# Optimization experiments

Measured on AMD Instinct MI355X. Metric: run time of the kernel, lower is better.

## Reference

```python
import jax, jax.numpy as jnp
import numpy as np

N = 100000       # nodes
E = 1600000      # edges (avg degree 16)
F_IN, H, C = 128, 128, 47


def setup_inputs() -> dict:
    key = jax.random.key(0)
    ks = jax.random.split(key, 12)
    def lin(k, fan_in, fan_out):
        return (jax.random.normal(k, (fan_in, fan_out), dtype=jnp.float32)
                / np.float32(np.sqrt(fan_in)))
    return {
        "x": jax.random.normal(ks[0], (N, F_IN), dtype=jnp.float32),
        "src": jax.random.randint(ks[1], (E,), 0, N, dtype=jnp.int32),
        "dst": jax.random.randint(ks[2], (E,), 0, N, dtype=jnp.int32),
        "w_self0": lin(ks[3], F_IN, H),
        "w_neigh0": lin(ks[4], F_IN, H),
        "b0": jnp.zeros((H,), jnp.float32),
        "w_self1": lin(ks[5], H, H),
        "w_neigh1": lin(ks[6], H, H),
        "b1": jnp.zeros((H,), jnp.float32),
        "w_self2": lin(ks[7], H, C),
        "w_neigh2": lin(ks[8], H, C),
        "b2": jnp.zeros((C,), jnp.float32),
    }


def _sage_layer(h, src, dst, w_self, w_neigh, b):
    # mean-aggregate neighbor features: gather h[src], scatter-add to dst
    agg = jax.ops.segment_sum(h[src], dst, num_segments=N)        # [N, d]
    deg = jax.ops.segment_sum(jnp.ones((src.shape[0], 1), h.dtype), dst,
                              num_segments=N)                     # [N, 1]
    mean = agg / jnp.maximum(deg, 1.0)
    # DGL SAGEConv('mean'): fc_self(h_dst) + fc_neigh(mean) + bias
    return h @ w_self + mean @ w_neigh + b


def reference(x, src, dst,
              w_self0, w_neigh0, b0,
              w_self1, w_neigh1, b1,
              w_self2, w_neigh2, b2):
    h = _sage_layer(x, src, dst, w_self0, w_neigh0, b0)
    h = jax.nn.relu(h)  # dropout is identity in eval mode
    h = _sage_layer(h, src, dst, w_self1, w_neigh1, b1)
    h = jax.nn.relu(h)
    h = _sage_layer(h, src, dst, w_self2, w_neigh2, b2)
    return h
```

## Files before the change

### kernel.cpp

```cpp
#include <hip/hip_runtime.h>

typedef unsigned int u32;
typedef unsigned short u16;
typedef __attribute__((ext_vector_type(8))) short short8;
typedef __attribute__((ext_vector_type(4))) float f32x4;

__device__ __forceinline__ u16 f2bf(float f) {
    u32 u = __float_as_uint(f);
    u32 r = (u + 0x7fffu + ((u >> 16) & 1u)) >> 16;
    return (u16)r;
}
__device__ __forceinline__ float bf2f(u32 lo16) { return __uint_as_float(lo16 << 16); }

__device__ __forceinline__ void acc_u4(float* a, uint4 v) {
    a[0] += bf2f(v.x & 0xffffu); a[1] += bf2f(v.x >> 16);
    a[2] += bf2f(v.y & 0xffffu); a[3] += bf2f(v.y >> 16);
    a[4] += bf2f(v.z & 0xffffu); a[5] += bf2f(v.z >> 16);
    a[6] += bf2f(v.w & 0xffffu); a[7] += bf2f(v.w >> 16);
}


__global__ __launch_bounds__(256) void prep_w_all(const float* __restrict__ ws0, const float* __restrict__ wn0, u16* __restrict__ wt0,
                                                  const float* __restrict__ ws1, const float* __restrict__ wn1, u16* __restrict__ wt1,
                                                  const float* __restrict__ ws2, const float* __restrict__ wn2, u16* __restrict__ wt2) {
    int bid = blockIdx.x;
    const float *ws, *wn;
    u16* wt;
    int dout, HW, local;
    if (bid < 128)      { ws = ws0; wn = wn0; wt = wt0; dout = 128; HW = 128; local = bid; }
    else if (bid < 256) { ws = ws1; wn = wn1; wt = wt1; dout = 128; HW = 128; local = bid - 128; }
    else                { ws = ws2; wn = wn2; wt = wt2; dout = 47;  HW = 64;  local = bid - 256; }
    int idx = local * 256 + threadIdx.x;
    int n = idx >> 7, k = idx & 127;
    float v = 0.f;
    if (n < HW) { if (n < dout) v = ws[k * dout + n]; }
    else { int nn = n - HW; if (nn < dout) v = wn[k * dout + nn]; }
    wt[idx] = f2bf(v);
}


__global__ __launch_bounds__(256) void hist_k(const int* __restrict__ dst,
                                              int* __restrict__ deg, int E) {
    int i = blockIdx.x * 256 + threadIdx.x;
    if (i < E) atomicAdd(&deg[dst[i]], 1);
}

__global__ __launch_bounds__(256) void scan_partial(const int* __restrict__ deg,
                                                    int* __restrict__ bsum, int Nn) {
    __shared__ int sm[256];
    int t = threadIdx.x;
    int base = blockIdx.x * 1024 + t * 4;
    int s = 0;
#pragma unroll
    for (int j = 0; j < 4; j++)
        if (base + j < Nn) s += deg[base + j];
    sm[t] = s;
    __syncthreads();
    for (int off = 128; off > 0; off >>= 1) {
        if (t < off) sm[t] += sm[t + off];
        __syncthreads();
    }
    if (t == 0) bsum[blockIdx.x] = sm[0];
}

__global__ __launch_bounds__(256) void scan_offsets(const int* __restrict__ bsum,
                                                    int* __restrict__ boff, int nb) {
    __shared__ int sm[256];
    int t = threadIdx.x;
    int v = (t < nb) ? bsum[t] : 0;
    sm[t] = v;
    __syncthreads();
    for (int off = 1; off < 256; off <<= 1) {
        int u = (t >= off) ? sm[t - off] : 0;
        __syncthreads();
        sm[t] += u;
        __syncthreads();
    }
    if (t < nb) boff[t] = sm[t] - v;
}

__global__ __launch_bounds__(1024) void scan_final(const int* __restrict__ deg,
                                                   const int* __restrict__ boff,
                                                   int* __restrict__ rowptr,
                                                   float* __restrict__ invd,
                                                   int* __restrict__ cursor,
                                                   int Nn, int E) {
    __shared__ int sm[1024];
    int t = threadIdx.x;
    int i = blockIdx.x * 1024 + t;
    int v = (i < Nn) ? deg[i] : 0;
    sm[t] = v;
    __syncthreads();
    for (int off = 1; off < 1024; off <<= 1) {
        int u = (t >= off) ? sm[t - off] : 0;
        __syncthreads();
        sm[t] += u;
        __syncthreads();
    }
    if (i < Nn) {
        int rp = boff[blockIdx.x] + sm[t] - v;
        rowptr[i] = rp;
        invd[i] = 1.0f / (float)max(v, 1);
        if ((i & 511) == 0) cursor[i >> 9] = rp;
    }
    if (i == Nn) rowptr[Nn] = E;
}

#define TILE 4096
__global__ __launch_bounds__(512) void bucket_scatter(const int* __restrict__ src,
                                                      const int* __restrict__ dst,
                                                      int* __restrict__ cursor,
                                                      uint2* __restrict__ pairs, int E) {
    __shared__ uint2 sp[TILE];
    __shared__ int s_cnt[256], s_off[256], s_gpos[256], s_cnt2[256];
    const int tid = threadIdx.x;
    const int base = blockIdx.x * TILE;
    const int tn = min(TILE, E - base);
    if (tid < 256) { s_cnt[tid] = 0; s_cnt2[tid] = 0; }
    __syncthreads();
    int d[8], s[8];
#pragma unroll
    for (int j = 0; j < 8; j++) {
        int k = tid + j * 512;
        if (k < tn) {
            d[j] = dst[base + k];
            s[j] = src[base + k];
            atomicAdd(&s_cnt[d[j] >> 9], 1);
        } else d[j] = -1;
    }
    __syncthreads();
    if (tid < 256) s_off[tid] = s_cnt[tid];
    __syncthreads();
    for (int off = 1; off < 256; off <<= 1) {
        int v = 0;
        if (tid < 256 && tid >= off) v = s_off[tid - off];
        __syncthreads();
        if (tid < 256) s_off[tid] += v;
        __syncthreads();
    }
    if (tid < 256 && s_cnt[tid] > 0) s_gpos[tid] = atomicAdd(&cursor[tid], s_cnt[tid]);
    __syncthreads();
#pragma unroll
    for (int j = 0; j < 8; j++) {
        if (d[j] >= 0) {
            int b = d[j] >> 9;
            int p = atomicAdd(&s_cnt2[b], 1);
            sp[s_off[b] - s_cnt[b] + p] = make_uint2((u32)d[j], (u32)s[j]);
        }
    }
    __syncthreads();
    for (int k = tid; k < tn; k += 512) {
        uint2 pr = sp[k];
        int b = (int)(pr.x >> 9);
        pairs[s_gpos[b] + (k - (s_off[b] - s_cnt[b]))] = pr;
    }
}

#define LDSCAP 12288
__global__ __launch_bounds__(512) void build_csr(const uint2* __restrict__ pairs,
                                                 const int* __restrict__ rowptr,
                                                 int* __restrict__ cols, int Nn) {
    __shared__ int s_cols[LDSCAP];
    __shared__ int s_row[513];
    __shared__ int s_cnt[512];
    const int tid = threadIdx.x;
    const int d0 = blockIdx.x * 512;
    const int nd = min(512, Nn - d0);
    for (int i = tid; i <= nd; i += 512) s_row[i] = rowptr[d0 + i];
    if (tid < nd) s_cnt[tid] = 0;
    __syncthreads();
    const int base = s_row[0];
    const int n = s_row[nd] - base;
    const bool fit = (n <= LDSCAP);
    for (int k = tid; k < n; k += 512) {
        uint2 pr = pairs[base + k];
        int dl = (int)pr.x - d0;
        int p = atomicAdd(&s_cnt[dl], 1);
        int pos = s_row[dl] - base + p;
        if (fit) s_cols[pos] = (int)pr.y;
        else cols[base + pos] = (int)pr.y;
    }
    __syncthreads();
    if (fit)
        for (int k = tid; k < n; k += 512) cols[base + k] = s_cols[k];
}

#define KDIM 128
#define KP 136

template <int NCOLS, bool AF32>
__global__ __launch_bounds__(256) void gemm_bf16(const void* __restrict__ Ap,
                                                 const u16* __restrict__ Bt,
                                                 u16* __restrict__ C, int M) {
    __shared__ u16 As[64 * KP];
    __shared__ u16 Bs[128 * KP];
    const int row0 = blockIdx.x * 64;
    const int col0 = blockIdx.y * 128;
    const int tid = threadIdx.x;

#pragma unroll
    for (int i = 0; i < 4; i++) {
        int idx = tid + i * 256;
        int r = idx >> 4, c = idx & 15;
        uint4 v = make_uint4(0, 0, 0, 0);
        if (row0 + r < M) {
            if (AF32) {
                const float* Af = (const float*)Ap;
                const float4* rowp = (const float4*)(Af + (size_t)(row0 + r) * KDIM);
                float4 f0 = rowp[2 * c];
                float4 f1 = rowp[2 * c + 1];
                v.x = (u32)f2bf(f0.x) | ((u32)f2bf(f0.y) << 16);
                v.y = (u32)f2bf(f0.z) | ((u32)f2bf(f0.w) << 16);
                v.z = (u32)f2bf(f1.x) | ((u32)f2bf(f1.y) << 16);
                v.w = (u32)f2bf(f1.z) | ((u32)f2bf(f1.w) << 16);
            } else {
                const u16* Ab = (const u16*)Ap;
                v = ((const uint4*)(Ab + (size_t)(row0 + r) * KDIM))[c];
            }
        }
        ((uint4*)(As + r * KP))[c] = v;
    }
#pragma unroll
    for (int i = 0; i < 8; i++) {
        int idx = tid + i * 256;
        int r = idx >> 4, c = idx & 15;
        uint4 v = ((const uint4*)(Bt + (size_t)(col0 + r) * KDIM))[c];
        ((uint4*)(Bs + r * KP))[c] = v;
    }
    __syncthreads();

    const int lane = tid & 63, wave = tid >> 6;
    const int quad = lane >> 4, l16 = lane & 15;
    const int wcol = wave * 32;

    f32x4 acc[4][2];
#pragma unroll
    for (int mt = 0; mt < 4; mt++)
#pragma unroll
        for (int nt = 0; nt < 2; nt++) acc[mt][nt] = (f32x4){0.f, 0.f, 0.f, 0.f};

#pragma unroll
    for (int kc = 0; kc < 4; kc++) {
        short8 a[4], b[2];
#pragma unroll
        for (int mt = 0; mt < 4; mt++)
            a[mt] = *(const short8*)(As + (size_t)(mt * 16 + l16) * KP + kc * 32 + quad * 8);
#pragma unroll
        for (int nt = 0; nt < 2; nt++)
            b[nt] = *(const short8*)(Bs + (size_t)(wcol + nt * 16 + l16) * KP + kc * 32 + quad * 8);
#pragma unroll
        for (int mt = 0; mt < 4; mt++)
#pragma unroll
            for (int nt = 0; nt < 2; nt++)
                acc[mt][nt] = __builtin_amdgcn_mfma_f32_16x16x32_bf16(a[mt], b[nt], acc[mt][nt], 0, 0, 0);
    }

    __syncthreads();
#pragma unroll
    for (int mt = 0; mt < 4; mt++)
#pragma unroll
        for (int i = 0; i < 4; i++) {
            int rl = mt * 16 + quad * 4 + i;
#pragma unroll
            for (int nt = 0; nt < 2; nt++)
                As[rl * KP + wcol + nt * 16 + l16] = f2bf(acc[mt][nt][i]);
        }
    __syncthreads();
#pragma unroll
    for (int it = 0; it < 4; it++) {
        int idx = tid + it * 256;
        int r = idx >> 4, c8 = idx & 15;
        if (row0 + r < M)
            *(uint4*)(C + (size_t)(row0 + r) * NCOLS + col0 + c8 * 8) =
                *(const uint4*)(As + r * KP + c8 * 8);
    }
}

template <bool RELU>
__global__ __launch_bounds__(256) void agg128_k(const u16* __restrict__ out2,
                                                const int* __restrict__ rowptr,
                                                const int* __restrict__ cols,
                                                const float* __restrict__ invd,
                                                const float* __restrict__ bias,
                                                u16* __restrict__ outp, int Mn) {
    int wave = threadIdx.x >> 6, lane = threadIdx.x & 63;
    int nA = blockIdx.x * 8 + wave * 2;
    if (nA >= Mn) return;
    const int nB = nA + 1;
    const bool hasB = (nB < Mn);
    int sub = lane >> 4, l16 = lane & 15;
    const u16* tb = out2 + 128 + 8 * l16;
    int begA = rowptr[nA], endA = rowptr[nA + 1];
    int begB = 0, endB = 0;
    if (hasB) { begB = rowptr[nB]; endB = rowptr[nB + 1]; }
    float aA[8] = {0.f, 0.f, 0.f, 0.f, 0.f, 0.f, 0.f, 0.f};
    float aB[8] = {0.f, 0.f, 0.f, 0.f, 0.f, 0.f, 0.f, 0.f};
    int eA = begA + sub, eB = begB + sub;
    while (eA < endA || eB < endB) {
        bool pA0 = eA < endA, pA1 = eA + 4 < endA;
        bool pB0 = eB < endB, pB1 = eB + 4 < endB;
        int sA0 = pA0 ? cols[eA] : 0;
        int sA1 = pA1 ? cols[eA + 4] : 0;
        int sB0 = pB0 ? cols[eB] : 0;
        int sB1 = pB1 ? cols[eB + 4] : 0;
        uint4 vA0 = *(const uint4*)(tb + (size_t)sA0 * 256);
        uint4 vA1 = *(const uint4*)(tb + (size_t)sA1 * 256);
        uint4 vB0 = *(const uint4*)(tb + (size_t)sB0 * 256);
        uint4 vB1 = *(const uint4*)(tb + (size_t)sB1 * 256);
        if (!pA0) vA0 = make_uint4(0, 0, 0, 0);
        if (!pA1) vA1 = make_uint4(0, 0, 0, 0);
        if (!pB0) vB0 = make_uint4(0, 0, 0, 0);
        if (!pB1) vB1 = make_uint4(0, 0, 0, 0);
        acc_u4(aA, vA0); acc_u4(aA, vA1);
        acc_u4(aB, vB0); acc_u4(aB, vB1);
        eA += 8; eB += 8;
    }
#pragma unroll
    for (int j = 0; j < 8; j++) {
        aA[j] += __shfl_xor(aA[j], 16); aA[j] += __shfl_xor(aA[j], 32);
        aB[j] += __shfl_xor(aB[j], 16); aB[j] += __shfl_xor(aB[j], 32);
    }
    if (sub == 0 || (sub == 1 && hasB)) {
        int node = (sub == 0) ? nA : nB;
        float o[8];
#pragma unroll
        for (int j = 0; j < 8; j++) o[j] = (sub == 0) ? aA[j] : aB[j];
        float id = invd[node];
        uint4 sv = *(const uint4*)(out2 + (size_t)node * 256 + 8 * l16);
        float4 b0 = *(const float4*)(bias + 8 * l16);
        float4 b1 = *(const float4*)(bias + 8 * l16 + 4);
        float o0 = bf2f(sv.x & 0xffffu) + o[0] * id + b0.x;
        float o1 = bf2f(sv.x >> 16)     + o[1] * id + b0.y;
        float o2 = bf2f(sv.y & 0xffffu) + o[2] * id + b0.z;
        float o3 = bf2f(sv.y >> 16)     + o[3] * id + b0.w;
        float o4 = bf2f(sv.z & 0xffffu) + o[4] * id + b1.x;
        float o5 = bf2f(sv.z >> 16)     + o[5] * id + b1.y;
        float o6 = bf2f(sv.w & 0xffffu) + o[6] * id + b1.z;
        float o7 = bf2f(sv.w >> 16)     + o[7] * id + b1.w;
        if (RELU) {
            o0 = fmaxf(o0, 0.f); o1 = fmaxf(o1, 0.f); o2 = fmaxf(o2, 0.f); o3 = fmaxf(o3, 0.f);
            o4 = fmaxf(o4, 0.f); o5 = fmaxf(o5, 0.f); o6 = fmaxf(o6, 0.f); o7 = fmaxf(o7, 0.f);
        }
        uint4 w;
        w.x = (u32)f2bf(o0) | ((u32)f2bf(o1) << 16);
        w.y = (u32)f2bf(o2) | ((u32)f2bf(o3) << 16);
        w.z = (u32)f2bf(o4) | ((u32)f2bf(o5) << 16);
        w.w = (u32)f2bf(o6) | ((u32)f2bf(o7) << 16);
        *(uint4*)(outp + (size_t)node * 128 + 8 * l16) = w;
    }
}

__global__ __launch_bounds__(256) void agg_out8_k(const u16* __restrict__ out2,
                                                  const int* __restrict__ rowptr,
                                                  const int* __restrict__ cols,
                                                  const float* __restrict__ invd,
                                                  const float* __restrict__ bias,
                                                  float* __restrict__ outp, int Mn) {
    int wave = threadIdx.x >> 6, lane = threadIdx.x & 63;
    int nA = blockIdx.x * 8 + wave * 2;
    if (nA >= Mn) return;
    const int nB = nA + 1;
    const bool hasB = (nB < Mn);
    int e8 = lane >> 3, l8 = lane & 7;
    const u16* tb = out2 + 64 + 8 * l8;
    int begA = rowptr[nA], endA = rowptr[nA + 1];
    int begB = 0, endB = 0;
    if (hasB) { begB = rowptr[nB]; endB = rowptr[nB + 1]; }
    float aA[8] = {0.f, 0.f, 0.f, 0.f, 0.f, 0.f, 0.f, 0.f};
    float aB[8] = {0.f, 0.f, 0.f, 0.f, 0.f, 0.f, 0.f, 0.f};
    int eA = begA + e8, eB = begB + e8;
    while (eA < endA || eB < endB) {
        bool pA0 = eA < endA, pA1 = eA + 8 < endA;
        bool pB0 = eB < endB, pB1 = eB + 8 < endB;
        int sA0 = pA0 ? cols[eA] : 0;
        int sA1 = pA1 ? cols[eA + 8] : 0;
        int sB0 = pB0 ? cols[eB] : 0;
        int sB1 = pB1 ? cols[eB + 8] : 0;
        uint4 vA0 = *(const uint4*)(tb + (size_t)sA0 * 128);
        uint4 vA1 = *(const uint4*)(tb + (size_t)sA1 * 128);
        uint4 vB0 = *(const uint4*)(tb + (size_t)sB0 * 128);
        uint4 vB1 = *(const uint4*)(tb + (size_t)sB1 * 128);
        if (!pA0) vA0 = make_uint4(0, 0, 0, 0);
        if (!pA1) vA1 = make_uint4(0, 0, 0, 0);
        if (!pB0) vB0 = make_uint4(0, 0, 0, 0);
        if (!pB1) vB1 = make_uint4(0, 0, 0, 0);
        acc_u4(aA, vA0); acc_u4(aA, vA1);
        acc_u4(aB, vB0); acc_u4(aB, vB1);
        eA += 16; eB += 16;
    }
#pragma unroll
    for (int j = 0; j < 8; j++) {
        aA[j] += __shfl_xor(aA[j], 8); aA[j] += __shfl_xor(aA[j], 16); aA[j] += __shfl_xor(aA[j], 32);
        aB[j] += __shfl_xor(aB[j], 8); aB[j] += __shfl_xor(aB[j], 16); aB[j] += __shfl_xor(aB[j], 32);
    }
    if (e8 == 0 || (e8 == 1 && hasB)) {
        int node = (e8 == 0) ? nA : nB;
        float o[8];
#pragma unroll
        for (int j = 0; j < 8; j++) o[j] = (e8 == 0) ? aA[j] : aB[j];
        float id = invd[node];
        uint4 sv = *(const uint4*)(out2 + (size_t)node * 128 + 8 * l8);
        u32 sw[4] = {sv.x, sv.y, sv.z, sv.w};
        float* orow = outp + (size_t)node * 47;
#pragma unroll
        for (int j = 0; j < 8; j++) {
            int c = 8 * l8 + j;
            if (c < 47) {
                float s = bf2f((j & 1) ? (sw[j >> 1] >> 16) : (sw[j >> 1] & 0xffffu));
                orow[c] = s + o[j] * id + bias[c];
            }
        }
    }
}


extern "C" void kernel_launch(void* const* d_in, const int* in_sizes, int n_in,
                              void* d_out, int out_size, void* d_ws, size_t ws_size,
                              hipStream_t stream) {
    const float* x   = (const float*)d_in[0];
    const int*   src = (const int*)d_in[1];
    const int*   dst = (const int*)d_in[2];
    const float* ws0 = (const float*)d_in[3];
    const float* wn0 = (const float*)d_in[4];
    const float* b0  = (const float*)d_in[5];
    const float* ws1 = (const float*)d_in[6];
    const float* wn1 = (const float*)d_in[7];
    const float* b1  = (const float*)d_in[8];
    const float* ws2 = (const float*)d_in[9];
    const float* wn2 = (const float*)d_in[10];
    const float* b2  = (const float*)d_in[11];

    const int Nn = in_sizes[0] / 128;
    const int E  = in_sizes[1];

    char* p = (char*)d_ws;
    auto alloc = [&](size_t bytes) -> void* {
        void* r = (void*)p;
        p += (bytes + 255) & ~(size_t)255;
        return r;
    };
    u16*   bufA   = (u16*)alloc((size_t)Nn * 128 * 2);
    u16*   out2   = (u16*)alloc((size_t)Nn * 256 * 2);
    u16*   wt0    = (u16*)alloc(256 * 128 * 2);
    u16*   wt1    = (u16*)alloc(256 * 128 * 2);
    u16*   wt2    = (u16*)alloc(128 * 128 * 2);
    int*   deg    = (int*)alloc((size_t)Nn * 4);
    int*   rowptr = (int*)alloc((size_t)(Nn + 1) * 4);
    float* invd   = (float*)alloc((size_t)Nn * 4);
    int*   cols   = (int*)alloc((size_t)E * 4);
    int*   bsum   = (int*)alloc(256 * 4);
    int*   boff   = (int*)alloc(256 * 4);
    int*   cursor = (int*)alloc(256 * 4);
    uint2* pairs  = (uint2*)out2;

    hipMemsetAsync(deg, 0, (size_t)Nn * 4, stream);

    prep_w_all<<<320, 256, 0, stream>>>(ws0, wn0, wt0, ws1, wn1, wt1, ws2, wn2, wt2);

    hist_k<<<(E + 255) / 256, 256, 0, stream>>>(dst, deg, E);
    const int nb = (Nn + 1023) / 1024;
    const int nb2 = (Nn + 1 + 1023) / 1024;
    scan_partial<<<nb, 256, 0, stream>>>(deg, bsum, Nn);
    scan_offsets<<<1, 256, 0, stream>>>(bsum, boff, nb);
    scan_final<<<nb2, 1024, 0, stream>>>(deg, boff, rowptr, invd, cursor, Nn, E);

    bucket_scatter<<<(E + TILE - 1) / TILE, 512, 0, stream>>>(src, dst, cursor, pairs, E);
    build_csr<<<(Nn + 511) / 512, 512, 0, stream>>>(pairs, rowptr, cols, Nn);

    dim3 ggrid((Nn + 63) / 64, 2);
    dim3 ggrid1((Nn + 63) / 64, 1);
    const int aggGrid = (Nn + 7) / 8;
    gemm_bf16<256, true><<<ggrid, 256, 0, stream>>>(x, wt0, out2, Nn);
    agg128_k<true><<<aggGrid, 256, 0, stream>>>(out2, rowptr, cols, invd, b0, bufA, Nn);
    gemm_bf16<256, false><<<ggrid, 256, 0, stream>>>(bufA, wt1, out2, Nn);
    agg128_k<true><<<aggGrid, 256, 0, stream>>>(out2, rowptr, cols, invd, b1, bufA, Nn);
    gemm_bf16<128, false><<<ggrid1, 256, 0, stream>>>(bufA, wt2, out2, Nn);
    agg_out8_k<<<aggGrid, 256, 0, stream>>>(out2, rowptr, cols, invd, b2, (float*)d_out, Nn);
}
```

Before: 448.8 us.

## Aggregate one node per wave with 4-deep gathers and zero sentinel row

The aggregation kernels now give each wave a single node instead of two, and unroll the edge loop to four gathers per lane per iteration. Out-of-range edges point to a zeroed sentinel row at index Mn, so the per-load predicate masking and the zeroing of loaded values go away. bf16-to-float unpacking is simplified with mask and shift pairs. The aim is more gathers in flight per lane and less branch and select overhead, at the cost of twice as many blocks, extra memsets, and fetching the sentinel row for low-degree nodes.

Result: no change. 451.7 us (+0.6%).

```diff
diff --git a/kernel.cpp b/kernel.cpp
--- a/kernel.cpp
+++ b/kernel.cpp
@@ -12,11 +12,16 @@
 }
 __device__ __forceinline__ float bf2f(u32 lo16) { return __uint_as_float(lo16 << 16); }
 
-__device__ __forceinline__ void acc_u4(float* a, uint4 v) {
-    a[0] += bf2f(v.x & 0xffffu); a[1] += bf2f(v.x >> 16);
-    a[2] += bf2f(v.y & 0xffffu); a[3] += bf2f(v.y >> 16);
-    a[4] += bf2f(v.z & 0xffffu); a[5] += bf2f(v.z >> 16);
-    a[6] += bf2f(v.w & 0xffffu); a[7] += bf2f(v.w >> 16);
+__device__ __forceinline__ void acc_u4p(float2* a, uint4 v) {
+    u32 w[4] = {v.x, v.y, v.z, v.w};
+#pragma unroll
+    for (int i = 0; i < 4; i++) {
+        float2 t;
+        t.x = __uint_as_float(w[i] << 16);
+        t.y = __uint_as_float(w[i] & 0xffff0000u);
+        a[i].x += t.x;
+        a[i].y += t.y;
+    }
 }
 
 
@@ -284,59 +289,45 @@
                                                 const float* __restrict__ bias,
                                                 u16* __restrict__ outp, int Mn) {
     int wave = threadIdx.x >> 6, lane = threadIdx.x & 63;
-    int nA = blockIdx.x * 8 + wave * 2;
-    if (nA >= Mn) return;
-    const int nB = nA + 1;
-    const bool hasB = (nB < Mn);
+    int node = blockIdx.x * 4 + wave;
+    if (node >= Mn) return;
     int sub = lane >> 4, l16 = lane & 15;
     const u16* tb = out2 + 128 + 8 * l16;
-    int begA = rowptr[nA], endA = rowptr[nA + 1];
-    int begB = 0, endB = 0;
-    if (hasB) { begB = rowptr[nB]; endB = rowptr[nB + 1]; }
-    float aA[8] = {0.f, 0.f, 0.f, 0.f, 0.f, 0.f, 0.f, 0.f};
-    float aB[8] = {0.f, 0.f, 0.f, 0.f, 0.f, 0.f, 0.f, 0.f};
-    int eA = begA + sub, eB = begB + sub;
-    while (eA < endA || eB < endB) {
-        bool pA0 = eA < endA, pA1 = eA + 4 < endA;
-        bool pB0 = eB < endB, pB1 = eB + 4 < endB;
-        int sA0 = pA0 ? cols[eA] : 0;
-        int sA1 = pA1 ? cols[eA + 4] : 0;
-        int sB0 = pB0 ? cols[eB] : 0;
-        int sB1 = pB1 ? cols[eB + 4] : 0;
-        uint4 vA0 = *(const uint4*)(tb + (size_t)sA0 * 256);
-        uint4 vA1 = *(const uint4*)(tb + (size_t)sA1 * 256);
-        uint4 vB0 = *(const uint4*)(tb + (size_t)sB0 * 256);
-        uint4 vB1 = *(const uint4*)(tb + (size_t)sB1 * 256);
-        if (!pA0) vA0 = make_uint4(0, 0, 0, 0);
-        if (!pA1) vA1 = make_uint4(0, 0, 0, 0);
-        if (!pB0) vB0 = make_uint4(0, 0, 0, 0);
-        if (!pB1) vB1 = make_uint4(0, 0, 0, 0);
-        acc_u4(aA, vA0); acc_u4(aA, vA1);
-        acc_u4(aB, vB0); acc_u4(aB, vB1);
-        eA += 8; eB += 8;
-    }
+    int beg = rowptr[node], end = rowptr[node + 1];
+    float2 a[4];
+#pragma unroll
+    for (int i = 0; i < 4; i++) a[i] = make_float2(0.f, 0.f);
+    int e = beg + sub;
+    while (e < end) {
+        int s0 = cols[e];
+        int s1 = (e + 4  < end) ? cols[e + 4]  : Mn;
+        int s2 = (e + 8  < end) ? cols[e + 8]  : Mn;
+        int s3 = (e + 12 < end) ? cols[e + 12] : Mn;
+        uint4 v0 = *(const uint4*)(tb + (size_t)s0 * 256);
+        uint4 v1 = *(const uint4*)(tb + (size_t)s1 * 256);
+        uint4 v2 = *(const uint4*)(tb + (size_t)s2 * 256);
+        uint4 v3 = *(const uint4*)(tb + (size_t)s3 * 256);
+        acc_u4p(a, v0); acc_u4p(a, v1); acc_u4p(a, v2); acc_u4p(a, v3);
+        e += 16;
+    }
+    float af[8] = {a[0].x, a[0].y, a[1].x, a[1].y, a[2].x, a[2].y, a[3].x, a[3].y};
 #pragma unroll
     for (int j = 0; j < 8; j++) {
-        aA[j] += __shfl_xor(aA[j], 16); aA[j] += __shfl_xor(aA[j], 32);
-        aB[j] += __shfl_xor(aB[j], 16); aB[j] += __shfl_xor(aB[j], 32);
-    }
-    if (sub == 0 || (sub == 1 && hasB)) {
-        int node = (sub == 0) ? nA : nB;
-        float o[8];
-#pragma unroll
-        for (int j = 0; j < 8; j++) o[j] = (sub == 0) ? aA[j] : aB[j];
+        af[j] += __shfl_xor(af[j], 16); af[j] += __shfl_xor(af[j], 32);
+    }
+    if (sub == 0) {
         float id = invd[node];
         uint4 sv = *(const uint4*)(out2 + (size_t)node * 256 + 8 * l16);
         float4 b0 = *(const float4*)(bias + 8 * l16);
         float4 b1 = *(const float4*)(bias + 8 * l16 + 4);
-        float o0 = bf2f(sv.x & 0xffffu) + o[0] * id + b0.x;
-        float o1 = bf2f(sv.x >> 16)     + o[1] * id + b0.y;
-        float o2 = bf2f(sv.y & 0xffffu) + o[2] * id + b0.z;
-        float o3 = bf2f(sv.y >> 16)     + o[3] * id + b0.w;
-        float o4 = bf2f(sv.z & 0xffffu) + o[4] * id + b1.x;
-        float o5 = bf2f(sv.z >> 16)     + o[5] * id + b1.y;
-        float o6 = bf2f(sv.w & 0xffffu) + o[6] * id + b1.z;
-        float o7 = bf2f(sv.w >> 16)     + o[7] * id + b1.w;
+        float o0 = bf2f(sv.x & 0xffffu) + af[0] * id + b0.x;
+        float o1 = bf2f(sv.x >> 16)     + af[1] * id + b0.y;
+        float o2 = bf2f(sv.y & 0xffffu) + af[2] * id + b0.z;
+        float o3 = bf2f(sv.y >> 16)     + af[3] * id + b0.w;
+        float o4 = bf2f(sv.z & 0xffffu) + af[4] * id + b1.x;
+        float o5 = bf2f(sv.z >> 16)     + af[5] * id + b1.y;
+        float o6 = bf2f(sv.w & 0xffffu) + af[6] * id + b1.z;
+        float o7 = bf2f(sv.w >> 16)     + af[7] * id + b1.w;
         if (RELU) {
             o0 = fmaxf(o0, 0.f); o1 = fmaxf(o1, 0.f); o2 = fmaxf(o2, 0.f); o3 = fmaxf(o3, 0.f);
             o4 = fmaxf(o4, 0.f); o5 = fmaxf(o5, 0.f); o6 = fmaxf(o6, 0.f); o7 = fmaxf(o7, 0.f);
@@ -357,47 +348,33 @@
                                                   const float* __restrict__ bias,
                                                   float* __restrict__ outp, int Mn) {
     int wave = threadIdx.x >> 6, lane = threadIdx.x & 63;
-    int nA = blockIdx.x * 8 + wave * 2;
-    if (nA >= Mn) return;
-    const int nB = nA + 1;
-    const bool hasB = (nB < Mn);
+    int node = blockIdx.x * 4 + wave;
+    if (node >= Mn) return;
     int e8 = lane >> 3, l8 = lane & 7;
     const u16* tb = out2 + 64 + 8 * l8;
-    int begA = rowptr[nA], endA = rowptr[nA + 1];
-    int begB = 0, endB = 0;
-    if (hasB) { begB = rowptr[nB]; endB = rowptr[nB + 1]; }
-    float aA[8] = {0.f, 0.f, 0.f, 0.f, 0.f, 0.f, 0.f, 0.f};
-    float aB[8] = {0.f, 0.f, 0.f, 0.f, 0.f, 0.f, 0.f, 0.f};
-    int eA = begA + e8, eB = begB + e8;
-    while (eA < endA || eB < endB) {
-        bool pA0 = eA < endA, pA1 = eA + 8 < endA;
-        bool pB0 = eB < endB, pB1 = eB + 8 < endB;
-        int sA0 = pA0 ? cols[eA] : 0;
-        int sA1 = pA1 ? cols[eA + 8] : 0;
-        int sB0 = pB0 ? cols[eB] : 0;
-        int sB1 = pB1 ? cols[eB + 8] : 0;
-        uint4 vA0 = *(const uint4*)(tb + (size_t)sA0 * 128);
-        uint4 vA1 = *(const uint4*)(tb + (size_t)sA1 * 128);
-        uint4 vB0 = *(const uint4*)(tb + (size_t)sB0 * 128);
-        uint4 vB1 = *(const uint4*)(tb + (size_t)sB1 * 128);
-        if (!pA0) vA0 = make_uint4(0, 0, 0, 0);
-        if (!pA1) vA1 = make_uint4(0, 0, 0, 0);
-        if (!pB0) vB0 = make_uint4(0, 0, 0, 0);
-        if (!pB1) vB1 = make_uint4(0, 0, 0, 0);
-        acc_u4(aA, vA0); acc_u4(aA, vA1);
-        acc_u4(aB, vB0); acc_u4(aB, vB1);
-        eA += 16; eB += 16;
-    }
+    int beg = rowptr[node], end = rowptr[node + 1];
+    float2 a[4];
+#pragma unroll
+    for (int i = 0; i < 4; i++) a[i] = make_float2(0.f, 0.f);
+    int e = beg + e8;
+    while (e < end) {
+        int s0 = cols[e];
+        int s1 = (e + 8  < end) ? cols[e + 8]  : Mn;
+        int s2 = (e + 16 < end) ? cols[e + 16] : Mn;
+        int s3 = (e + 24 < end) ? cols[e + 24] : Mn;
+        uint4 v0 = *(const uint4*)(tb + (size_t)s0 * 128);
+        uint4 v1 = *(const uint4*)(tb + (size_t)s1 * 128);
+        uint4 v2 = *(const uint4*)(tb + (size_t)s2 * 128);
+        uint4 v3 = *(const uint4*)(tb + (size_t)s3 * 128);
+        acc_u4p(a, v0); acc_u4p(a, v1); acc_u4p(a, v2); acc_u4p(a, v3);
+        e += 32;
+    }
+    float af[8] = {a[0].x, a[0].y, a[1].x, a[1].y, a[2].x, a[2].y, a[3].x, a[3].y};
 #pragma unroll
     for (int j = 0; j < 8; j++) {
-        aA[j] += __shfl_xor(aA[j], 8); aA[j] += __shfl_xor(aA[j], 16); aA[j] += __shfl_xor(aA[j], 32);
-        aB[j] += __shfl_xor(aB[j], 8); aB[j] += __shfl_xor(aB[j], 16); aB[j] += __shfl_xor(aB[j], 32);
-    }
-    if (e8 == 0 || (e8 == 1 && hasB)) {
-        int node = (e8 == 0) ? nA : nB;
-        float o[8];
-#pragma unroll
-        for (int j = 0; j < 8; j++) o[j] = (e8 == 0) ? aA[j] : aB[j];
+        af[j] += __shfl_xor(af[j], 8); af[j] += __shfl_xor(af[j], 16); af[j] += __shfl_xor(af[j], 32);
+    }
+    if (e8 == 0) {
         float id = invd[node];
         uint4 sv = *(const uint4*)(out2 + (size_t)node * 128 + 8 * l8);
         u32 sw[4] = {sv.x, sv.y, sv.z, sv.w};
@@ -407,7 +384,7 @@
             int c = 8 * l8 + j;
             if (c < 47) {
                 float s = bf2f((j & 1) ? (sw[j >> 1] >> 16) : (sw[j >> 1] & 0xffffu));
-                orow[c] = s + o[j] * id + bias[c];
+                orow[c] = s + af[j] * id + bias[c];
             }
         }
     }
@@ -440,20 +417,21 @@
         return r;
     };
     u16*   bufA   = (u16*)alloc((size_t)Nn * 128 * 2);
-    u16*   out2   = (u16*)alloc((size_t)Nn * 256 * 2);
+    u16*   out2   = (u16*)alloc(((size_t)Nn * 256 + 256) * 2);
     u16*   wt0    = (u16*)alloc(256 * 128 * 2);
     u16*   wt1    = (u16*)alloc(256 * 128 * 2);
     u16*   wt2    = (u16*)alloc(128 * 128 * 2);
     int*   deg    = (int*)alloc((size_t)Nn * 4);
     int*   rowptr = (int*)alloc((size_t)(Nn + 1) * 4);
     float* invd   = (float*)alloc((size_t)Nn * 4);
-    int*   cols   = (int*)alloc((size_t)E * 4);
+    int*   cols   = (int*)alloc((size_t)(E + 32) * 4);
     int*   bsum   = (int*)alloc(256 * 4);
     int*   boff   = (int*)alloc(256 * 4);
     int*   cursor = (int*)alloc(256 * 4);
     uint2* pairs  = (uint2*)out2;
 
     hipMemsetAsync(deg, 0, (size_t)Nn * 4, stream);
+    hipMemsetAsync(out2 + (size_t)Nn * 256, 0, 512, stream);
 
     prep_w_all<<<320, 256, 0, stream>>>(ws0, wn0, wt0, ws1, wn1, wt1, ws2, wn2, wt2);
 
@@ -469,11 +447,12 @@
 
     dim3 ggrid((Nn + 63) / 64, 2);
     dim3 ggrid1((Nn + 63) / 64, 1);
-    const int aggGrid = (Nn + 7) / 8;
+    const int aggGrid = (Nn + 3) / 4;
     gemm_bf16<256, true><<<ggrid, 256, 0, stream>>>(x, wt0, out2, Nn);
     agg128_k<true><<<aggGrid, 256, 0, stream>>>(out2, rowptr, cols, invd, b0, bufA, Nn);
     gemm_bf16<256, false><<<ggrid, 256, 0, stream>>>(bufA, wt1, out2, Nn);
     agg128_k<true><<<aggGrid, 256, 0, stream>>>(out2, rowptr, cols, invd, b1, bufA, Nn);
     gemm_bf16<128, false><<<ggrid1, 256, 0, stream>>>(bufA, wt2, out2, Nn);
+    hipMemsetAsync(out2 + (size_t)Nn * 128, 0, 256, stream);
     agg_out8_k<<<aggGrid, 256, 0, stream>>>(out2, rowptr, cols, invd, b2, (float*)d_out, Nn);
 }
```
